# Performance work log

Measured on AMD Instinct MI355X. Metric: run time of the kernel, lower is better.

Reference implementation:

```python
import jax, jax.numpy as jnp
import numpy as np

EPS = 1e-12  # F.normalize default eps

def _l2norm(x, axis):
    n = jnp.sqrt(jnp.sum(x * x, axis=axis, keepdims=True))
    return x / jnp.maximum(n, EPS)

def setup_inputs() -> dict:
    key = jax.random.key(0)
    k1, k2 = jax.random.split(key)
    B, S, H, L = 64, 1024, 1024, 3
    deep_features = jax.random.normal(k1, (B, S, H), dtype=jnp.float32)
    label_embeddings = jax.random.normal(k2, (H, L), dtype=jnp.float32)
    attention_mask = jnp.ones((B, S), dtype=jnp.float32)
    return {"deep_features": deep_features,
            "label_embeddings": label_embeddings,
            "attention_mask": attention_mask}

def reference(deep_features, label_embeddings, attention_mask):
    # L2-normalize features over hidden dim, labels over hidden (dim=0)
    df_n = _l2norm(deep_features, axis=-1)              # [B,S,H]
    le_n = _l2norm(label_embeddings, axis=0)            # [H,L]
    atten = jnp.einsum('bsh,hl->bsl', df_n, le_n)       # [B,S,L]
    # additive mask bias: 10000*(mask-1), broadcast over L
    bias = 10000.0 * (attention_mask - 1.0)             # [B,S]
    atten = atten + bias[:, :, None]                    # [B,S,L]
    # MaxPool1d(kernel=3, stride=3) over L; L==3 -> single window, then squeeze
    pooled = jnp.max(atten, axis=-1)                    # [B,S]
    normalized = jax.nn.softmax(pooled, axis=1)         # softmax over seq dim
    # weighted sum of features: [B,1,S] @ [B,S,H] -> [B,H]
    feature_attention = jnp.einsum('bs,bsh->bh', normalized, deep_features)
    return (feature_attention, atten, normalized[:, None, :])
```

## Files before the change

### kernel.cpp

```cpp
#include <hip/hip_runtime.h>
#include <math.h>

constexpr int B = 64;
constexpr int S = 1024;
constexpr int H = 1024;
constexpr int L = 3;
#define NEPS 1e-12f

__device__ __forceinline__ float wave_reduce_sum(float v) {
    #pragma unroll
    for (int off = 32; off > 0; off >>= 1) v += __shfl_xor(v, off);
    return v;
}
__device__ __forceinline__ float wave_reduce_max(float v) {
    #pragma unroll
    for (int off = 32; off > 0; off >>= 1) v = fmaxf(v, __shfl_xor(v, off));
    return v;
}

__global__ __launch_bounds__(256) void norm_labels(const float* __restrict__ le,
                                                   float* __restrict__ leT) {
    __shared__ float red[L][4];
    __shared__ float rn[L];
    const int tid = threadIdx.x;
    const int wid = tid >> 6, lane = tid & 63;

    float acc[L] = {0.f, 0.f, 0.f};
    for (int h = tid; h < H; h += 256) {
        #pragma unroll
        for (int l = 0; l < L; ++l) {
            float v = le[h * L + l];
            acc[l] += v * v;
        }
    }
    #pragma unroll
    for (int l = 0; l < L; ++l) {
        float s = wave_reduce_sum(acc[l]);
        if (lane == 0) red[l][wid] = s;
    }
    __syncthreads();
    if (tid < L) {
        float s = red[tid][0] + red[tid][1] + red[tid][2] + red[tid][3];
        rn[tid] = 1.0f / fmaxf(sqrtf(s), NEPS);
    }
    __syncthreads();
    for (int h = tid; h < H; h += 256) {
        #pragma unroll
        for (int l = 0; l < L; ++l)
            leT[l * H + h] = le[h * L + l] * rn[l];
    }
}

__global__ __launch_bounds__(256) void row_kernel(const float* __restrict__ df,
                                                  const float* __restrict__ leT,
                                                  const float* __restrict__ mask,
                                                  float* __restrict__ atten,
                                                  float* __restrict__ pooled) {
    const int wid = threadIdx.x >> 6, lane = threadIdx.x & 63;
    const int row = blockIdx.x * 4 + wid;
    const float* r = df + (size_t)row * H;

    float ssq = 0.f, d0 = 0.f, d1 = 0.f, d2 = 0.f;
    #pragma unroll
    for (int k = 0; k < 4; ++k) {
        const int idx = (k * 64 + lane) * 4;
        const float4 d  = *(const float4*)(r + idx);
        const float4 a0 = *(const float4*)(leT + 0 * H + idx);
        const float4 a1 = *(const float4*)(leT + 1 * H + idx);
        const float4 a2 = *(const float4*)(leT + 2 * H + idx);
        ssq += d.x * d.x  + d.y * d.y  + d.z * d.z  + d.w * d.w;
        d0  += d.x * a0.x + d.y * a0.y + d.z * a0.z + d.w * a0.w;
        d1  += d.x * a1.x + d.y * a1.y + d.z * a1.z + d.w * a1.w;
        d2  += d.x * a2.x + d.y * a2.y + d.z * a2.z + d.w * a2.w;
    }
    #pragma unroll
    for (int off = 32; off > 0; off >>= 1) {
        ssq += __shfl_xor(ssq, off);
        d0  += __shfl_xor(d0, off);
        d1  += __shfl_xor(d1, off);
        d2  += __shfl_xor(d2, off);
    }
    if (lane == 0) {
        const float rnrm = 1.0f / fmaxf(sqrtf(ssq), NEPS);
        const float bias = 10000.0f * (mask[row] - 1.0f);
        const float v0 = d0 * rnrm + bias;
        const float v1 = d1 * rnrm + bias;
        const float v2 = d2 * rnrm + bias;
        float* o = atten + (size_t)row * L;
        o[0] = v0; o[1] = v1; o[2] = v2;
        pooled[row] = fmaxf(fmaxf(v0, v1), v2);
    }
}

__global__ __launch_bounds__(256) void softmax_kernel(const float* __restrict__ pooled,
                                                      float* __restrict__ norm,
                                                      float* __restrict__ fa) {
    const int b = blockIdx.x;
    const int tid = threadIdx.x;
    const int wid = tid >> 6, lane = tid & 63;

    *(float4*)(fa + (size_t)b * H + tid * 4) = make_float4(0.f, 0.f, 0.f, 0.f);

    const float4 p = *(const float4*)(pooled + (size_t)b * S + tid * 4);

    __shared__ float redm[4];
    __shared__ float reds[4];
    float m = fmaxf(fmaxf(p.x, p.y), fmaxf(p.z, p.w));
    m = wave_reduce_max(m);
    if (lane == 0) redm[wid] = m;
    __syncthreads();
    m = fmaxf(fmaxf(redm[0], redm[1]), fmaxf(redm[2], redm[3]));

    float4 e;
    e.x = expf(p.x - m);
    e.y = expf(p.y - m);
    e.z = expf(p.z - m);
    e.w = expf(p.w - m);
    float ssum = e.x + e.y + e.z + e.w;
    ssum = wave_reduce_sum(ssum);
    if (lane == 0) reds[wid] = ssum;
    __syncthreads();
    const float rs = 1.0f / (reds[0] + reds[1] + reds[2] + reds[3]);

    e.x *= rs; e.y *= rs; e.z *= rs; e.w *= rs;
    *(float4*)(norm + (size_t)b * S + tid * 4) = e;
}

constexpr int SCHUNK = 32;
__global__ __launch_bounds__(256) void weighted_sum(const float* __restrict__ df,
                                                    const float* __restrict__ norm,
                                                    float* __restrict__ fa) {
    const int c = blockIdx.x;
    const int b = blockIdx.y;
    const int tid = threadIdx.x;

    __shared__ float w[SCHUNK];
    if (tid < SCHUNK) w[tid] = norm[(size_t)b * S + c * SCHUNK + tid];
    __syncthreads();

    const float* base = df + ((size_t)b * S + (size_t)c * SCHUNK) * H + tid * 4;
    float4 acc = make_float4(0.f, 0.f, 0.f, 0.f);
    #pragma unroll 8
    for (int i = 0; i < SCHUNK; ++i) {
        const float4 d = *(const float4*)(base + (size_t)i * H);
        const float ww = w[i];
        acc.x += ww * d.x;
        acc.y += ww * d.y;
        acc.z += ww * d.z;
        acc.w += ww * d.w;
    }
    float* o = fa + (size_t)b * H + tid * 4;
    atomicAdd(o + 0, acc.x);
    atomicAdd(o + 1, acc.y);
    atomicAdd(o + 2, acc.z);
    atomicAdd(o + 3, acc.w);
}

extern "C" void kernel_launch(void* const* d_in, const int* in_sizes, int n_in,
                              void* d_out, int out_size, void* d_ws, size_t ws_size,
                              hipStream_t stream) {
    const float* df   = (const float*)d_in[0];
    const float* le   = (const float*)d_in[1];
    const float* mask = (const float*)d_in[2];

    float* out   = (float*)d_out;
    float* fa    = out;
    float* atten = out + (size_t)B * H;
    float* norm  = atten + (size_t)B * S * L;

    float* leT    = (float*)d_ws;
    float* pooled = leT + (size_t)L * H;

    norm_labels<<<1, 256, 0, stream>>>(le, leT);
    row_kernel<<<(B * S) / 4, 256, 0, stream>>>(df, leT, mask, atten, pooled);
    softmax_kernel<<<B, 256, 0, stream>>>(pooled, norm, fa);
    weighted_sum<<<dim3(S / SCHUNK, B), 256, 0, stream>>>(df, norm, fa);
}
```

Measured before the change: 403.8 us.

## Fuse row scoring with online-softmax weighted sum in single pass over features

Merges the per-row normalize/score kernel with the weighted-sum pass using an online softmax (running max and rescaled accumulator). The 256MB feature tensor is read once instead of twice. Each wave keeps partial sums over 16 rows and writes them out, and a small epilogue kernel merges the partials and computes the normalized weights. This removes the atomics and one kernel launch. In exchange, each row goes through a serial dependency chain inside its wave, only 1024 blocks are launched so there is less parallelism in flight, and the accumulators use more registers.

```diff
diff --git a/kernel.cpp b/kernel.cpp
--- a/kernel.cpp
+++ b/kernel.cpp
@@ -5,6 +5,8 @@
 constexpr int S = 1024;
 constexpr int H = 1024;
 constexpr int L = 3;
+constexpr int WPB = 64;
+constexpr int RPW = S / WPB;
 #define NEPS 1e-12f
 
 __device__ __forceinline__ float wave_reduce_sum(float v) {
@@ -51,109 +53,146 @@
     }
 }
 
-__global__ __launch_bounds__(256) void row_kernel(const float* __restrict__ df,
-                                                  const float* __restrict__ leT,
-                                                  const float* __restrict__ mask,
-                                                  float* __restrict__ atten,
-                                                  float* __restrict__ pooled) {
+__global__ __launch_bounds__(256) void fused_stream(const float* __restrict__ df,
+                                                    const float* __restrict__ leT,
+                                                    const float* __restrict__ mask,
+                                                    float* __restrict__ atten,
+                                                    float* __restrict__ pooled,
+                                                    float* __restrict__ accp,
+                                                    float* __restrict__ mz) {
     const int wid = threadIdx.x >> 6, lane = threadIdx.x & 63;
-    const int row = blockIdx.x * 4 + wid;
-    const float* r = df + (size_t)row * H;
-
-    float ssq = 0.f, d0 = 0.f, d1 = 0.f, d2 = 0.f;
+    const int gw = blockIdx.x * 4 + wid;
+    const int b = gw / WPB;
+    const int j = gw % WPB;
+    const int s0 = j * RPW;
+
+    float4 L0[4], L1[4], L2[4];
     #pragma unroll
     for (int k = 0; k < 4; ++k) {
         const int idx = (k * 64 + lane) * 4;
-        const float4 d  = *(const float4*)(r + idx);
-        const float4 a0 = *(const float4*)(leT + 0 * H + idx);
-        const float4 a1 = *(const float4*)(leT + 1 * H + idx);
-        const float4 a2 = *(const float4*)(leT + 2 * H + idx);
-        ssq += d.x * d.x  + d.y * d.y  + d.z * d.z  + d.w * d.w;
-        d0  += d.x * a0.x + d.y * a0.y + d.z * a0.z + d.w * a0.w;
-        d1  += d.x * a1.x + d.y * a1.y + d.z * a1.z + d.w * a1.w;
-        d2  += d.x * a2.x + d.y * a2.y + d.z * a2.z + d.w * a2.w;
-    }
-    #pragma unroll
-    for (int off = 32; off > 0; off >>= 1) {
-        ssq += __shfl_xor(ssq, off);
-        d0  += __shfl_xor(d0, off);
-        d1  += __shfl_xor(d1, off);
-        d2  += __shfl_xor(d2, off);
-    }
-    if (lane == 0) {
+        L0[k] = *(const float4*)(leT + 0 * H + idx);
+        L1[k] = *(const float4*)(leT + 1 * H + idx);
+        L2[k] = *(const float4*)(leT + 2 * H + idx);
+    }
+
+    float4 acc[4];
+    #pragma unroll
+    for (int k = 0; k < 4; ++k) acc[k] = make_float4(0.f, 0.f, 0.f, 0.f);
+    float m = -INFINITY, Z = 0.f;
+
+    for (int i = 0; i < RPW; ++i) {
+        const int row = b * S + s0 + i;
+        const float* r = df + (size_t)row * H;
+        float4 d[4];
+        #pragma unroll
+        for (int k = 0; k < 4; ++k)
+            d[k] = *(const float4*)(r + (k * 64 + lane) * 4);
+
+        float ssq = 0.f, d0 = 0.f, d1 = 0.f, d2 = 0.f;
+        #pragma unroll
+        for (int k = 0; k < 4; ++k) {
+            ssq += d[k].x * d[k].x   + d[k].y * d[k].y   + d[k].z * d[k].z   + d[k].w * d[k].w;
+            d0  += d[k].x * L0[k].x  + d[k].y * L0[k].y  + d[k].z * L0[k].z  + d[k].w * L0[k].w;
+            d1  += d[k].x * L1[k].x  + d[k].y * L1[k].y  + d[k].z * L1[k].z  + d[k].w * L1[k].w;
+            d2  += d[k].x * L2[k].x  + d[k].y * L2[k].y  + d[k].z * L2[k].z  + d[k].w * L2[k].w;
+        }
+        #pragma unroll
+        for (int off = 32; off > 0; off >>= 1) {
+            ssq += __shfl_xor(ssq, off);
+            d0  += __shfl_xor(d0, off);
+            d1  += __shfl_xor(d1, off);
+            d2  += __shfl_xor(d2, off);
+        }
+
         const float rnrm = 1.0f / fmaxf(sqrtf(ssq), NEPS);
         const float bias = 10000.0f * (mask[row] - 1.0f);
         const float v0 = d0 * rnrm + bias;
         const float v1 = d1 * rnrm + bias;
         const float v2 = d2 * rnrm + bias;
-        float* o = atten + (size_t)row * L;
-        o[0] = v0; o[1] = v1; o[2] = v2;
-        pooled[row] = fmaxf(fmaxf(v0, v1), v2);
-    }
-}
-
-__global__ __launch_bounds__(256) void softmax_kernel(const float* __restrict__ pooled,
-                                                      float* __restrict__ norm,
-                                                      float* __restrict__ fa) {
+        const float p  = fmaxf(fmaxf(v0, v1), v2);
+        if (lane == 0) {
+            float* o = atten + (size_t)row * L;
+            o[0] = v0; o[1] = v1; o[2] = v2;
+            pooled[row] = p;
+        }
+
+        if (p > m) {
+            const float sc = __expf(m - p);
+            Z *= sc;
+            #pragma unroll
+            for (int k = 0; k < 4; ++k) {
+                acc[k].x *= sc; acc[k].y *= sc; acc[k].z *= sc; acc[k].w *= sc;
+            }
+            m = p;
+        }
+        const float e = __expf(p - m);
+        Z += e;
+        #pragma unroll
+        for (int k = 0; k < 4; ++k) {
+            acc[k].x += e * d[k].x;
+            acc[k].y += e * d[k].y;
+            acc[k].z += e * d[k].z;
+            acc[k].w += e * d[k].w;
+        }
+    }
+
+    float* ap = accp + ((size_t)b * WPB + j) * H;
+    #pragma unroll
+    for (int k = 0; k < 4; ++k)
+        *(float4*)(ap + (k * 64 + lane) * 4) = acc[k];
+    if (lane == 0) {
+        mz[((size_t)b * WPB + j) * 2 + 0] = m;
+        mz[((size_t)b * WPB + j) * 2 + 1] = Z;
+    }
+}
+
+__global__ __launch_bounds__(256) void epilogue(const float* __restrict__ accp,
+                                                const float* __restrict__ mz,
+                                                const float* __restrict__ pooled,
+                                                float* __restrict__ norm,
+                                                float* __restrict__ fa) {
     const int b = blockIdx.x;
     const int tid = threadIdx.x;
-    const int wid = tid >> 6, lane = tid & 63;
-
-    *(float4*)(fa + (size_t)b * H + tid * 4) = make_float4(0.f, 0.f, 0.f, 0.f);
-
-    const float4 p = *(const float4*)(pooled + (size_t)b * S + tid * 4);
-
-    __shared__ float redm[4];
-    __shared__ float reds[4];
-    float m = fmaxf(fmaxf(p.x, p.y), fmaxf(p.z, p.w));
-    m = wave_reduce_max(m);
-    if (lane == 0) redm[wid] = m;
-    __syncthreads();
-    m = fmaxf(fmaxf(redm[0], redm[1]), fmaxf(redm[2], redm[3]));
-
-    float4 e;
-    e.x = expf(p.x - m);
-    e.y = expf(p.y - m);
-    e.z = expf(p.z - m);
-    e.w = expf(p.w - m);
-    float ssum = e.x + e.y + e.z + e.w;
-    ssum = wave_reduce_sum(ssum);
-    if (lane == 0) reds[wid] = ssum;
-    __syncthreads();
-    const float rs = 1.0f / (reds[0] + reds[1] + reds[2] + reds[3]);
-
-    e.x *= rs; e.y *= rs; e.z *= rs; e.w *= rs;
-    *(float4*)(norm + (size_t)b * S + tid * 4) = e;
-}
-
-constexpr int SCHUNK = 32;
-__global__ __launch_bounds__(256) void weighted_sum(const float* __restrict__ df,
-                                                    const float* __restrict__ norm,
-                                                    float* __restrict__ fa) {
-    const int c = blockIdx.x;
-    const int b = blockIdx.y;
-    const int tid = threadIdx.x;
-
-    __shared__ float w[SCHUNK];
-    if (tid < SCHUNK) w[tid] = norm[(size_t)b * S + c * SCHUNK + tid];
-    __syncthreads();
-
-    const float* base = df + ((size_t)b * S + (size_t)c * SCHUNK) * H + tid * 4;
-    float4 acc = make_float4(0.f, 0.f, 0.f, 0.f);
+
+    __shared__ float sM, sZ;
+    __shared__ float ew[WPB];
+
+    float mj = 0.f, zj = 0.f;
+    if (tid < WPB) {
+        const float2 p = *(const float2*)(mz + ((size_t)b * WPB + tid) * 2);
+        mj = p.x; zj = p.y;
+        float M = wave_reduce_max(mj);
+        if (tid == 0) sM = M;
+    }
+    __syncthreads();
+    const float M = sM;
+    if (tid < WPB) {
+        const float e = __expf(mj - M);
+        ew[tid] = e;
+        float z = wave_reduce_sum(zj * e);
+        if (tid == 0) sZ = z;
+    }
+    __syncthreads();
+    const float rZ = 1.0f / sZ;
+
+    const float* ap = accp + (size_t)b * WPB * H + tid * 4;
+    float4 a = make_float4(0.f, 0.f, 0.f, 0.f);
     #pragma unroll 8
-    for (int i = 0; i < SCHUNK; ++i) {
-        const float4 d = *(const float4*)(base + (size_t)i * H);
-        const float ww = w[i];
-        acc.x += ww * d.x;
-        acc.y += ww * d.y;
-        acc.z += ww * d.z;
-        acc.w += ww * d.w;
-    }
-    float* o = fa + (size_t)b * H + tid * 4;
-    atomicAdd(o + 0, acc.x);
-    atomicAdd(o + 1, acc.y);
-    atomicAdd(o + 2, acc.z);
-    atomicAdd(o + 3, acc.w);
+    for (int j = 0; j < WPB; ++j) {
+        const float4 v = *(const float4*)(ap + (size_t)j * H);
+        const float w = ew[j];
+        a.x += w * v.x; a.y += w * v.y; a.z += w * v.z; a.w += w * v.w;
+    }
+    a.x *= rZ; a.y *= rZ; a.z *= rZ; a.w *= rZ;
+    *(float4*)(fa + (size_t)b * H + tid * 4) = a;
+
+    const float4 p4 = *(const float4*)(pooled + (size_t)b * S + tid * 4);
+    float4 n4;
+    n4.x = __expf(p4.x - M) * rZ;
+    n4.y = __expf(p4.y - M) * rZ;
+    n4.z = __expf(p4.z - M) * rZ;
+    n4.w = __expf(p4.w - M) * rZ;
+    *(float4*)(norm + (size_t)b * S + tid * 4) = n4;
 }
 
 extern "C" void kernel_launch(void* const* d_in, const int* in_sizes, int n_in,
@@ -170,9 +209,10 @@
 
     float* leT    = (float*)d_ws;
     float* pooled = leT + (size_t)L * H;
+    float* mz     = pooled + (size_t)B * S;
+    float* accp   = mz + (size_t)B * WPB * 2;
 
     norm_labels<<<1, 256, 0, stream>>>(le, leT);
-    row_kernel<<<(B * S) / 4, 256, 0, stream>>>(df, leT, mask, atten, pooled);
-    softmax_kernel<<<B, 256, 0, stream>>>(pooled, norm, fa);
-    weighted_sum<<<dim3(S / SCHUNK, B), 256, 0, stream>>>(df, norm, fa);
-}
+    fused_stream<<<(B * WPB) / 4, 256, 0, stream>>>(df, leT, mask, atten, pooled, accp, mz);
+    epilogue<<<B, 256, 0, stream>>>(accp, mz, pooled, norm, fa);
+}
```

After: 370.1 us. 1.09x faster.
